# Kernel tuning notes

Hardware: AMD Instinct MI355X
Metric: run time of the kernel (lower is better)

The kernel has to match this reference:

```python
import jax, jax.numpy as jnp
import numpy as np

D = 500  # GRUCell hidden/input size (hardcoded in source)


def setup_inputs() -> dict:
    key = jax.random.key(0)
    k1, k2, k3, k4, k5 = jax.random.split(key, 5)
    B = 512
    bound = 1.0 / np.sqrt(D)  # torch GRUCell default uniform init bound
    state = jax.random.normal(k1, (B, D), dtype=jnp.float32)
    W_ih = jax.random.uniform(k2, (3 * D, D), jnp.float32, -bound, bound)
    W_hh = jax.random.uniform(k3, (3 * D, D), jnp.float32, -bound, bound)
    b_ih = jax.random.uniform(k4, (3 * D,), jnp.float32, -bound, bound)
    b_hh = jax.random.uniform(k5, (3 * D,), jnp.float32, -bound, bound)
    break_condition = jnp.float32(0.9)  # nn.Parameter(torch.tensor(0.9))
    recursion_limit = 64  # source uses 10000; reduced for a runnable baseline
    return {
        "state": state, "W_ih": W_ih, "W_hh": W_hh,
        "b_ih": b_ih, "b_hh": b_hh,
        "break_condition": break_condition,
        "recursion_limit": recursion_limit,
    }


def _gru_cell(x, h, W_ih, W_hh, b_ih, b_hh):
    # torch.nn.GRUCell math
    gi = x @ W_ih.T + b_ih          # [B, 3D]
    gh = h @ W_hh.T + b_hh          # [B, 3D]
    i_r, i_z, i_n = jnp.split(gi, 3, axis=-1)
    h_r, h_z, h_n = jnp.split(gh, 3, axis=-1)
    r = jax.nn.sigmoid(i_r + h_r)
    z = jax.nn.sigmoid(i_z + h_z)
    n = jnp.tanh(i_n + r * h_n)
    return (1.0 - z) * n + z * h


def reference(state, W_ih, W_hh, b_ih, b_hh, break_condition, recursion_limit):
    h0 = jnp.zeros_like(state)

    def step(carry, _):
        s, h, done = carry
        h_new = _gru_cell(s, h, W_ih, W_hh, b_ih, b_hh)
        done_new = done | (jnp.mean(h_new) > break_condition)
        # latch state/hidden once the break condition has fired
        s_out = jnp.where(done, s, h_new)
        h_out = jnp.where(done, h, h_new)
        return (s_out, h_out, done_new), None

    init = (state, h0, jnp.array(False))
    (s_fin, _, _), _ = jax.lax.scan(step, init, None, length=recursion_limit)
    return s_fin
```

## Files before the change

### kernel.cpp

```cpp
#include <hip/hip_runtime.h>
#include <math.h>
#include <stdint.h>

#define DD 500
#define BB 512
#define NSTRIPS 64
#define MSTRIPS 16
#define WKSTEPS 96
#define AKSTEPS 64
#define NELEM (BB*DD)
#define GM 16
#define GN 8
#define NBLK 128
#define HSTRIDE 2048

typedef _Float16 f16;
typedef _Float16 f16x8 __attribute__((ext_vector_type(8)));
typedef float    f32x16 __attribute__((ext_vector_type(16)));
typedef unsigned u32x4  __attribute__((ext_vector_type(4)));

#define APCNT ((size_t)MSTRIPS * AKSTEPS * 64 * 8)
#define WPCNT ((size_t)NSTRIPS * WKSTEPS * 64 * 8)


__device__ __forceinline__ float aload_f32(const float* p) {
    return __hip_atomic_load(p, __ATOMIC_RELAXED, __HIP_MEMORY_SCOPE_AGENT);
}
__device__ __forceinline__ void aload16i(u32x4& d, const f16* p) {
    asm volatile("global_load_dwordx4 %0, %1, off sc0 sc1"
                 : "=&v"(d) : "v"(p) : "memory");
}
__device__ __forceinline__ void astore16(f16* p, u32x4 v) {
    asm volatile("global_store_dwordx4 %0, %1, off sc0 sc1"
                 :: "v"(p), "v"(v) : "memory");
}

__device__ __forceinline__ float fsigmoid(float x) {
    return 1.0f / (1.0f + __expf(-x));
}
__device__ __forceinline__ float ftanh(float x) {
    return 2.0f / (1.0f + __expf(-2.0f * x)) - 1.0f;
}

__global__ __launch_bounds__(256) void conv_w(const float* __restrict__ Wih,
                                              const float* __restrict__ Whh,
                                              f16* __restrict__ Wp0,
                                              f16* __restrict__ Wp1)
{
    int p = blockIdx.x * 256 + threadIdx.x;
    const int ln = p & 63; p >>= 6;
    const int kstep = p % WKSTEPS;
    const int strip = p / WKSTEPS;
    const int q = ln & 31;
    const int g = q >> 3;
    const int d = strip * 8 + (q & 7);
    const int kb0 = kstep * 16 + (ln >> 5) * 8;
    const int blk = kb0 >> 9, bk0 = kb0 & 511;
    const float* pih = 0;
    const float* phh = 0;
    if (d < DD) {
        if (g == 0)      { pih = Wih + (size_t)d * DD;
                           phh = Whh + (size_t)d * DD; }
        else if (g == 1) { pih = Wih + (size_t)(500 + d) * DD;
                           phh = Whh + (size_t)(500 + d) * DD; }
        else if (g == 2) { pih = Wih + (size_t)(1000 + d) * DD; }
        else             { phh = Whh + (size_t)(1000 + d) * DD; }
    }
    f16 o0[8], o1[8];
    #pragma unroll
    for (int j = 0; j < 8; ++j) {
        const int bk = bk0 + j;
        float vi = 0.f, vh = 0.f;
        if (bk < DD) {
            if (pih) vi = pih[bk];
            if (phh) vh = phh[bk];
        }
        const float v0 = (g == 3) ? vh : vi;
        const float v1 = (g <= 1) ? (vi + vh) : v0;
        f16 h0 = (f16)v0;
        f16 h1 = (f16)v1;
        o0[j] = (blk == 2) ? (f16)(v0 - (float)h0) : h0;
        o1[j] = (blk == 2) ? (f16)(v1 - (float)h1) : h1;
    }
    const size_t off = ((size_t)(strip * WKSTEPS + kstep) * 64 + ln) * 8;
    *(uint4*)(Wp0 + off) = *(uint4*)o0;
    *(uint4*)(Wp1 + off) = *(uint4*)o1;
}

__global__ __launch_bounds__(256) void conv_a(const float* __restrict__ S,
                                              f16* __restrict__ Ap)
{
    int p = blockIdx.x * 256 + threadIdx.x;
    const int ln = p & 63; p >>= 6;
    const int kstep = p % AKSTEPS;
    const int strip = p / AKSTEPS;
    const int b = strip * 32 + (ln & 31);
    const int kb0 = kstep * 16 + (ln >> 5) * 8;
    const int blk = kb0 >> 9, bk0 = kb0 & 511;
    f16 out[8];
    #pragma unroll
    for (int j = 0; j < 8; ++j) {
        const int bk = bk0 + j;
        float v = (bk < DD) ? S[(size_t)b * DD + bk] : 0.f;
        f16 hi = (f16)v;
        out[j] = (blk == 1) ? (f16)(v - (float)hi) : hi;
    }
    *(uint4*)(Ap + ((size_t)(strip * AKSTEPS + kstep) * 64 + ln) * 8) = *(uint4*)out;
}

__device__ __forceinline__ void grid_sync(unsigned* bar, unsigned e)
{
    __syncthreads();
    if (threadIdx.x == 0) {
        unsigned* gcnt = bar + ((blockIdx.x >> 3) << 4);
        unsigned* root = bar + 512;
        unsigned* gen  = bar + 528;
        unsigned a = __hip_atomic_fetch_add(gcnt, 1u, __ATOMIC_RELAXED,
                                            __HIP_MEMORY_SCOPE_AGENT);
        if (a == e * 8u + 7u) {
            unsigned r = __hip_atomic_fetch_add(root, 1u, __ATOMIC_RELAXED,
                                                __HIP_MEMORY_SCOPE_AGENT);
            if (r == e * 16u + 15u) {
                __hip_atomic_store(gen, e + 1u, __ATOMIC_RELAXED,
                                   __HIP_MEMORY_SCOPE_AGENT);
            } else {
                while (__hip_atomic_load(gen, __ATOMIC_RELAXED,
                                         __HIP_MEMORY_SCOPE_AGENT) <= e)
                    __builtin_amdgcn_s_sleep(1);
            }
        } else {
            while (__hip_atomic_load(gen, __ATOMIC_RELAXED,
                                     __HIP_MEMORY_SCOPE_AGENT) <= e)
                __builtin_amdgcn_s_sleep(1);
        }
    }
    __syncthreads();
}

__global__ __launch_bounds__(512, 2) void gru_persist(
    f16* __restrict__ ApB,
    const f16* __restrict__ Wp0, const f16* __restrict__ Wp1,
    const float* __restrict__ bih, const float* __restrict__ bhh,
    float* __restrict__ out, float* __restrict__ spart,
    const float* __restrict__ bc, const int* __restrict__ rec,
    unsigned* __restrict__ bar, unsigned* __restrict__ garr,
    float* __restrict__ hist)
{
    const int bid = blockIdx.x;
    const int tid = threadIdx.x;
    const int rounds = min(64, rec[0]);
    if (rounds <= 0) return;
    const float thr = bc[0] * (float)NELEM;

    const int cg = bid & 7;
    const int mg = bid >> 3;
    const int wv = tid >> 6, ln = tid & 63;
    const int pp = wv & 3;
    const int kh = wv >> 2;
    const int ks0 = kh * 48;
    const int sb0 = cg * 8 + 2 * pp, sb1 = sb0 + 1;

    __shared__ __align__(16) char smem[65536];
    f16*      Alds  = (f16*)smem;
    float*    Ct    = (float*)smem;
    unsigned* hbufP = (unsigned*)(smem + 40960);
    float*    red   = (float*)(smem + 49408);
    int*      trig  = (int*)(smem + 49440);

    float h[4];
    #pragma unroll
    for (int i = 0; i < 4; ++i) h[i] = 0.0f;

    f16* bufs0 = ApB;
    f16* bufs1 = ApB + APCNT;
    unsigned* gptr = garr + mg * 16;
    unsigned wep = 0;

    for (int t = 0; t < rounds; ++t) {
        const f16* Wb   = (t == 0) ? Wp0 : Wp1;
        const f16* Bp0  = Wb + (size_t)(sb0 * WKSTEPS + ks0) * 512 + (size_t)ln * 8;
        const f16* Bp1  = Wb + (size_t)(sb1 * WKSTEPS + ks0) * 512 + (size_t)ln * 8;
        const f16* Asrc = ((t & 1) ? bufs1 : bufs0) + (size_t)mg * AKSTEPS * 512;
        f16*       Apw  = ((t & 1) ? bufs0 : bufs1);

        uint4 rB0[12], rB1[12];
        #pragma unroll
        for (int i = 0; i < 12; ++i) {
            rB0[i] = *(const uint4*)(Bp0 + (size_t)i * 512);
            rB1[i] = *(const uint4*)(Bp1 + (size_t)i * 512);
        }
        if (t > 0) {
            if (tid == 0) {
                while (__hip_atomic_load(gptr, __ATOMIC_RELAXED,
                                         __HIP_MEMORY_SCOPE_AGENT)
                       < 8u * (unsigned)t)
                    __builtin_amdgcn_s_sleep(1);
            }
            __syncthreads();
        }

        {
            u32x4 av[8];
            #pragma unroll
            for (int i = 0; i < 8; ++i)
                aload16i(av[i], Asrc + (size_t)(tid + 512 * i) * 8);
            asm volatile("s_waitcnt vmcnt(0)" ::: "memory");
            __builtin_amdgcn_sched_barrier(0);
            #pragma unroll
            for (int i = 0; i < 8; ++i)
                *(u32x4*)(Alds + (size_t)(tid + 512 * i) * 8) = av[i];
        }
        __syncthreads();

        f32x16 acc0 = {}, acc1 = {};
        #pragma unroll
        for (int ksl = 0; ksl < 48; ++ksl) {
            const int ks = ks0 + ksl;
            const int kr = (ks < 64) ? ks : (ks - 64);
            f16x8 a = *(const f16x8*)(Alds + (size_t)(kr * 64 + ln) * 8);
            acc0 = __builtin_amdgcn_mfma_f32_32x32x16_f16(
                       a, *(f16x8*)&rB0[ksl % 12], acc0, 0, 0, 0);
            acc1 = __builtin_amdgcn_mfma_f32_32x32x16_f16(
                       a, *(f16x8*)&rB1[ksl % 12], acc1, 0, 0, 0);
            if (ksl < 36) {
                rB0[ksl % 12] = *(const uint4*)(Bp0 + (size_t)(ksl + 12) * 512);
                rB1[ksl % 12] = *(const uint4*)(Bp1 + (size_t)(ksl + 12) * 512);
            }
        }
        __syncthreads();

        {
            const int q = ln & 31, g = q >> 3, dd = q & 7;
            const int sl0 = 2 * pp, sl1 = 2 * pp + 1;
            if (kh == 0) {
                #pragma unroll
                for (int r = 0; r < 16; ++r) {
                    const int row = (r & 3) + 8 * (r >> 2) + 4 * (ln >> 5);
                    Ct[row * 288 + sl0 * 36 + g * 9 + dd] = acc0[r];
                    Ct[row * 288 + sl1 * 36 + g * 9 + dd] = acc1[r];
                }
            }
            __syncthreads();
            if (kh == 1) {
                #pragma unroll
                for (int r = 0; r < 16; ++r) {
                    const int row = (r & 3) + 8 * (r >> 2) + 4 * (ln >> 5);
                    Ct[row * 288 + sl0 * 36 + g * 9 + dd] += acc0[r];
                    Ct[row * 288 + sl1 * 36 + g * 9 + dd] += acc1[r];
                }
            }
            __syncthreads();
        }

        float* hw = hist + ((size_t)bid * 8 + (size_t)(t & 7)) * HSTRIDE;
        float psum = 0.0f;
        #pragma unroll
        for (int i = 0; i < 4; ++i) {
            const int idx = i * 512 + tid;
            const int row = idx >> 6, dl = idx & 63;
            const int d = cg * 64 + dl;
            const int sl = dl >> 3, dd = dl & 7;
            float hnew = 0.0f;
            if (d < DD) {
                const float* cb = &Ct[row * 288 + sl * 36 + dd];
                float cr = cb[0], cz = cb[9], cin = cb[18], chn = cb[27];
                float r = fsigmoid(cr + bih[d] + bhh[d]);
                float z = fsigmoid(cz + bih[500 + d] + bhh[500 + d]);
                float inn = cin + bih[1000 + d];
                float hn  = bhh[1000 + d];
                float hp  = 0.0f;
                if (t > 0) { hn += chn; hp = h[i]; }
                float n = ftanh(inn + r * hn);
                hnew = (1.0f - z) * n + z * hp;
                psum += hnew;
            }
            h[i] = hnew;
            hw[idx] = hnew;
            f16 hi = (f16)hnew;
            f16 lo = (f16)(hnew - (float)hi);
            union { f16 f[2]; unsigned u; } pk;
            pk.f[0] = hi; pk.f[1] = lo;
            hbufP[row * 65 + dl] = pk.u;
        }
        #pragma unroll
        for (int off = 32; off > 0; off >>= 1) psum += __shfl_down(psum, off, 64);
        if (ln == 0) red[wv] = psum;
        __syncthreads();
        if (tid == 0) {
            float v = red[0] + red[1] + red[2] + red[3]
                    + red[4] + red[5] + red[6] + red[7];
            __hip_atomic_fetch_add(&spart[(size_t)cg * 64 + t], v,
                                   __ATOMIC_RELAXED, __HIP_MEMORY_SCOPE_AGENT);
        }
        if (tid < 256) {
            const int lm = tid & 31, oct = tid >> 5;
            union { f16 a[8]; u32x4 v; } hiU, loU;
            #pragma unroll
            for (int j = 0; j < 8; ++j) {
                unsigned u = hbufP[lm * 65 + oct * 8 + j];
                union { unsigned u; f16 f[2]; } pk; pk.u = u;
                hiU.a[j] = pk.f[0];
                loU.a[j] = pk.f[1];
            }
            const int kst = cg * 4 + (oct >> 1), half = oct & 1;
            f16* dhi = Apw + ((size_t)(mg * AKSTEPS + kst)      * 64 + half * 32 + lm) * 8;
            f16* dlo = Apw + ((size_t)(mg * AKSTEPS + 32 + kst) * 64 + half * 32 + lm) * 8;
            astore16(dhi, hiU.v);
            astore16(dlo, loU.v);
        }
        asm volatile("s_waitcnt vmcnt(0)" ::: "memory");
        __syncthreads();
        if (tid == 0)
            __hip_atomic_fetch_add(gptr, 1u, __ATOMIC_RELAXED,
                                   __HIP_MEMORY_SCOPE_AGENT);

        if (((t & 7) == 7) || (t == rounds - 1)) {
            grid_sync(bar, wep++);
            if (tid < 64) {
                const int cgl = tid & 7, ti = tid >> 3;
                const int tt = (t & ~7) + ti;
                float v = 0.f;
                if (tt <= t)
                    v = aload_f32(&spart[(size_t)cgl * 64 + tt]);
                v += __shfl_xor(v, 1, 64);
                v += __shfl_xor(v, 2, 64);
                v += __shfl_xor(v, 4, 64);
                bool hit = ((tid & 7) == 0) && (tt <= t) && (v > thr);
                unsigned long long m = __ballot(hit);
                if (tid == 0)
                    trig[0] = m ? (int)((__ffsll((long long)m) - 1) >> 3) : -1;
            }
            __syncthreads();
            const int w0 = trig[0];
            if (w0 >= 0) {
                const int ts = (t & ~7) + w0;
                const float* hs = hist
                    + ((size_t)bid * 8 + (size_t)(ts & 7)) * HSTRIDE;
                #pragma unroll
                for (int i = 0; i < 4; ++i) {
                    const int idx = i * 512 + tid;
                    const int row = idx >> 6, dl = idx & 63;
                    const int d = cg * 64 + dl;
                    if (d < DD)
                        out[(size_t)(mg * 32 + row) * DD + d] = hs[idx];
                }
                return;
            }
        }
    }

    #pragma unroll
    for (int i = 0; i < 4; ++i) {
        const int idx = i * 512 + tid;
        const int row = idx >> 6, dl = idx & 63;
        const int d = cg * 64 + dl;
        if (d < DD)
            out[(size_t)(mg * 32 + row) * DD + d] = h[i];
    }
}

extern "C" void kernel_launch(void* const* d_in, const int* in_sizes, int n_in,
                              void* d_out, int out_size, void* d_ws, size_t ws_size,
                              hipStream_t stream)
{
    const float* state = (const float*)d_in[0];
    const float* Wih   = (const float*)d_in[1];
    const float* Whh   = (const float*)d_in[2];
    const float* bih   = (const float*)d_in[3];
    const float* bhh   = (const float*)d_in[4];
    const float* bc    = (const float*)d_in[5];
    const int*   rec   = (const int*)d_in[6];

    char* ws = (char*)d_ws;
    float*    spart = (float*)ws;
    unsigned* bar   = (unsigned*)(ws + 2048);
    unsigned* garr  = (unsigned*)(ws + 6144);
    f16*   ApB   = (f16*)(ws + 8192);
    f16*   Wp0   = ApB + 2 * APCNT;
    f16*   Wp1   = Wp0 + WPCNT;
    float* hist  = (float*)(Wp1 + WPCNT);
    float* out   = (float*)d_out;

    hipMemsetAsync(ws, 0, 8192, stream);
    hipMemcpyAsync(out, state, (size_t)NELEM * sizeof(float),
                   hipMemcpyDeviceToDevice, stream);

    conv_w<<<dim3(NSTRIPS * WKSTEPS * 64 / 256), 256, 0, stream>>>(Wih, Whh, Wp0, Wp1);
    conv_a<<<dim3(MSTRIPS * AKSTEPS * 64 / 256), 256, 0, stream>>>(state, ApB);

    gru_persist<<<dim3(NBLK), dim3(512), 0, stream>>>(
        ApB, Wp0, Wp1, bih, bhh, out, spart, bc, rec, bar, garr, hist);
}
```

Measured before the change: 803.4 us.

## Repartition persistent GRU grid to 256 blocks with 64-row by 16-column tiles

Changes the persistent kernel's work split from 128 blocks (32 rows × 64 hidden columns, K split in two halves) to 256 blocks (64 rows × 16 hidden columns, K split four ways across waves). Each block now keeps fewer weight strips in registers and loads its A operand in two staged halves through LDS, overlapping the second half's global load with the first half's MFMAs. The aim is to put more CUs to work per recurrent step and shorten per-step latency. The cost is a wider grid barrier and row-group counter (32 arrivals instead of 8), four serialized LDS reduction passes, and more duplicated A traffic per block.

```diff
diff --git a/kernel.cpp b/kernel.cpp
--- a/kernel.cpp
+++ b/kernel.cpp
@@ -9,10 +9,10 @@
 #define WKSTEPS 96
 #define AKSTEPS 64
 #define NELEM (BB*DD)
-#define GM 16
-#define GN 8
-#define NBLK 128
-#define HSTRIDE 2048
+#define GRG 8
+#define GCG 32
+#define NBLK 256
+#define HSTRIDE 1024
 
 typedef _Float16 f16;
 typedef _Float16 f16x8 __attribute__((ext_vector_type(8)));
@@ -120,7 +120,7 @@
         if (a == e * 8u + 7u) {
             unsigned r = __hip_atomic_fetch_add(root, 1u, __ATOMIC_RELAXED,
                                                 __HIP_MEMORY_SCOPE_AGENT);
-            if (r == e * 16u + 15u) {
+            if (r == e * 32u + 31u) {
                 __hip_atomic_store(gen, e + 1u, __ATOMIC_RELAXED,
                                    __HIP_MEMORY_SCOPE_AGENT);
             } else {
@@ -152,117 +152,146 @@
     if (rounds <= 0) return;
     const float thr = bc[0] * (float)NELEM;
 
-    const int cg = bid & 7;
-    const int mg = bid >> 3;
+    const int cg = bid & 31;
+    const int rg = bid >> 5;
     const int wv = tid >> 6, ln = tid & 63;
-    const int pp = wv & 3;
-    const int kh = wv >> 2;
-    const int ks0 = kh * 48;
-    const int sb0 = cg * 8 + 2 * pp, sb1 = sb0 + 1;
+    const int mh = wv >> 2;
+    const int kq = wv & 3;
+    const int sb0 = cg * 2, sb1 = cg * 2 + 1;
 
     __shared__ __align__(16) char smem[65536];
     f16*      Alds  = (f16*)smem;
     float*    Ct    = (float*)smem;
-    unsigned* hbufP = (unsigned*)(smem + 40960);
-    float*    red   = (float*)(smem + 49408);
-    int*      trig  = (int*)(smem + 49440);
-
-    float h[4];
-    #pragma unroll
-    for (int i = 0; i < 4; ++i) h[i] = 0.0f;
+    unsigned* hbufP = (unsigned*)(smem + 20480);
+    float*    red   = (float*)(smem + 24832);
+    int*      trig  = (int*)(smem + 24864);
+
+    float h[2];
+    h[0] = 0.0f; h[1] = 0.0f;
 
     f16* bufs0 = ApB;
     f16* bufs1 = ApB + APCNT;
-    unsigned* gptr = garr + mg * 16;
+    unsigned* gptr = garr + rg * 16;
     unsigned wep = 0;
 
     for (int t = 0; t < rounds; ++t) {
-        const f16* Wb   = (t == 0) ? Wp0 : Wp1;
-        const f16* Bp0  = Wb + (size_t)(sb0 * WKSTEPS + ks0) * 512 + (size_t)ln * 8;
-        const f16* Bp1  = Wb + (size_t)(sb1 * WKSTEPS + ks0) * 512 + (size_t)ln * 8;
-        const f16* Asrc = ((t & 1) ? bufs1 : bufs0) + (size_t)mg * AKSTEPS * 512;
-        f16*       Apw  = ((t & 1) ? bufs0 : bufs1);
-
-        uint4 rB0[12], rB1[12];
-        #pragma unroll
-        for (int i = 0; i < 12; ++i) {
-            rB0[i] = *(const uint4*)(Bp0 + (size_t)i * 512);
-            rB1[i] = *(const uint4*)(Bp1 + (size_t)i * 512);
+        const f16* Wb    = (t == 0) ? Wp0 : Wp1;
+        const f16* Abase = (t & 1) ? bufs1 : bufs0;
+        f16*       Apw   = (t & 1) ? bufs0 : bufs1;
+        const f16* Bb0   = Wb + (size_t)sb0 * WKSTEPS * 512 + (size_t)ln * 8;
+        const f16* Bb1   = Wb + (size_t)sb1 * WKSTEPS * 512 + (size_t)ln * 8;
+
+        uint4 rB0[8], rB1[8];
+        #pragma unroll
+        for (int i = 0; i < 8; ++i) {
+            rB0[i] = *(const uint4*)(Bb0 + (size_t)(kq * 8 + i) * 512);
+            rB1[i] = *(const uint4*)(Bb1 + (size_t)(kq * 8 + i) * 512);
         }
         if (t > 0) {
             if (tid == 0) {
                 while (__hip_atomic_load(gptr, __ATOMIC_RELAXED,
                                          __HIP_MEMORY_SCOPE_AGENT)
-                       < 8u * (unsigned)t)
+                       < 32u * (unsigned)t)
                     __builtin_amdgcn_s_sleep(1);
             }
             __syncthreads();
         }
 
-        {
-            u32x4 av[8];
-            #pragma unroll
-            for (int i = 0; i < 8; ++i)
-                aload16i(av[i], Asrc + (size_t)(tid + 512 * i) * 8);
-            asm volatile("s_waitcnt vmcnt(0)" ::: "memory");
-            __builtin_amdgcn_sched_barrier(0);
-            #pragma unroll
-            for (int i = 0; i < 8; ++i)
-                *(u32x4*)(Alds + (size_t)(tid + 512 * i) * 8) = av[i];
+        u32x4 av[8];
+        #pragma unroll
+        for (int i = 0; i < 8; ++i) {
+            const int flat = tid + 512 * i;
+            const int sl_ = flat >> 11, rem = flat & 2047;
+            aload16i(av[i], Abase +
+                ((size_t)((2 * rg + sl_) * AKSTEPS + (rem >> 6)) * 64
+                 + (rem & 63)) * 8);
+        }
+        asm volatile("s_waitcnt vmcnt(0)" ::: "memory");
+        __builtin_amdgcn_sched_barrier(0);
+        #pragma unroll
+        for (int i = 0; i < 8; ++i)
+            *(u32x4*)(Alds + (size_t)(tid + 512 * i) * 8) = av[i];
+        #pragma unroll
+        for (int i = 0; i < 8; ++i) {
+            const int flat = tid + 512 * i;
+            const int sl_ = flat >> 11, rem = flat & 2047;
+            aload16i(av[i], Abase +
+                ((size_t)((2 * rg + sl_) * AKSTEPS + 32 + (rem >> 6)) * 64
+                 + (rem & 63)) * 8);
         }
         __syncthreads();
 
         f32x16 acc0 = {}, acc1 = {};
         #pragma unroll
-        for (int ksl = 0; ksl < 48; ++ksl) {
-            const int ks = ks0 + ksl;
-            const int kr = (ks < 64) ? ks : (ks - 64);
-            f16x8 a = *(const f16x8*)(Alds + (size_t)(kr * 64 + ln) * 8);
+        for (int ksl = 0; ksl < 16; ++ksl) {
+            const int ka = kq * 8 + (ksl & 7);
+            f16x8 a = *(const f16x8*)(Alds + ((size_t)(mh * 32 + ka) * 512
+                                              + (size_t)ln * 8));
             acc0 = __builtin_amdgcn_mfma_f32_32x32x16_f16(
-                       a, *(f16x8*)&rB0[ksl % 12], acc0, 0, 0, 0);
+                       a, *(f16x8*)&rB0[ksl & 7], acc0, 0, 0, 0);
             acc1 = __builtin_amdgcn_mfma_f32_32x32x16_f16(
-                       a, *(f16x8*)&rB1[ksl % 12], acc1, 0, 0, 0);
-            if (ksl < 36) {
-                rB0[ksl % 12] = *(const uint4*)(Bp0 + (size_t)(ksl + 12) * 512);
-                rB1[ksl % 12] = *(const uint4*)(Bp1 + (size_t)(ksl + 12) * 512);
-            }
+                       a, *(f16x8*)&rB1[ksl & 7], acc1, 0, 0, 0);
+            if (ksl < 8) {
+                rB0[ksl] = *(const uint4*)(Bb0 + (size_t)(64 + kq * 8 + ksl) * 512);
+                rB1[ksl] = *(const uint4*)(Bb1 + (size_t)(64 + kq * 8 + ksl) * 512);
+            }
+        }
+        __syncthreads();
+
+        asm volatile("s_waitcnt vmcnt(0)" ::: "memory");
+        __builtin_amdgcn_sched_barrier(0);
+        #pragma unroll
+        for (int i = 0; i < 8; ++i)
+            *(u32x4*)(Alds + (size_t)(tid + 512 * i) * 8) = av[i];
+        #pragma unroll
+        for (int i = 0; i < 8; ++i) {
+            rB0[i] = *(const uint4*)(Bb0 + (size_t)(32 + kq * 8 + i) * 512);
+            rB1[i] = *(const uint4*)(Bb1 + (size_t)(32 + kq * 8 + i) * 512);
+        }
+        __syncthreads();
+
+        #pragma unroll
+        for (int ksl = 0; ksl < 8; ++ksl) {
+            const int ka = kq * 8 + ksl;
+            f16x8 a = *(const f16x8*)(Alds + ((size_t)(mh * 32 + ka) * 512
+                                              + (size_t)ln * 8));
+            acc0 = __builtin_amdgcn_mfma_f32_32x32x16_f16(
+                       a, *(f16x8*)&rB0[ksl], acc0, 0, 0, 0);
+            acc1 = __builtin_amdgcn_mfma_f32_32x32x16_f16(
+                       a, *(f16x8*)&rB1[ksl], acc1, 0, 0, 0);
         }
         __syncthreads();
 
         {
             const int q = ln & 31, g = q >> 3, dd = q & 7;
-            const int sl0 = 2 * pp, sl1 = 2 * pp + 1;
-            if (kh == 0) {
-                #pragma unroll
-                for (int r = 0; r < 16; ++r) {
-                    const int row = (r & 3) + 8 * (r >> 2) + 4 * (ln >> 5);
-                    Ct[row * 288 + sl0 * 36 + g * 9 + dd] = acc0[r];
-                    Ct[row * 288 + sl1 * 36 + g * 9 + dd] = acc1[r];
+            #pragma unroll
+            for (int k = 0; k < 4; ++k) {
+                if (kq == k) {
+                    #pragma unroll
+                    for (int r = 0; r < 16; ++r) {
+                        const int row = mh * 32 + (r & 3) + 8 * (r >> 2)
+                                        + 4 * (ln >> 5);
+                        float* c0 = Ct + row * 72 + g * 9 + dd;
+                        float* c1 = c0 + 36;
+                        if (k == 0) { *c0 = acc0[r];  *c1 = acc1[r]; }
+                        else        { *c0 += acc0[r]; *c1 += acc1[r]; }
+                    }
                 }
-            }
-            __syncthreads();
-            if (kh == 1) {
-                #pragma unroll
-                for (int r = 0; r < 16; ++r) {
-                    const int row = (r & 3) + 8 * (r >> 2) + 4 * (ln >> 5);
-                    Ct[row * 288 + sl0 * 36 + g * 9 + dd] += acc0[r];
-                    Ct[row * 288 + sl1 * 36 + g * 9 + dd] += acc1[r];
-                }
-            }
-            __syncthreads();
+                __syncthreads();
+            }
         }
 
         float* hw = hist + ((size_t)bid * 8 + (size_t)(t & 7)) * HSTRIDE;
         float psum = 0.0f;
         #pragma unroll
-        for (int i = 0; i < 4; ++i) {
+        for (int i = 0; i < 2; ++i) {
             const int idx = i * 512 + tid;
-            const int row = idx >> 6, dl = idx & 63;
-            const int d = cg * 64 + dl;
+            const int row = idx >> 4, dl = idx & 15;
+            const int d = cg * 16 + dl;
             const int sl = dl >> 3, dd = dl & 7;
             float hnew = 0.0f;
             if (d < DD) {
-                const float* cb = &Ct[row * 288 + sl * 36 + dd];
+                const float* cb = &Ct[row * 72 + sl * 36 + dd];
                 float cr = cb[0], cz = cb[9], cin = cb[18], chn = cb[27];
                 float r = fsigmoid(cr + bih[d] + bhh[d]);
                 float z = fsigmoid(cz + bih[500 + d] + bhh[500 + d]);
@@ -280,7 +309,7 @@
             f16 lo = (f16)(hnew - (float)hi);
             union { f16 f[2]; unsigned u; } pk;
             pk.f[0] = hi; pk.f[1] = lo;
-            hbufP[row * 65 + dl] = pk.u;
+            hbufP[row * 17 + dl] = pk.u;
         }
         #pragma unroll
         for (int off = 32; off > 0; off >>= 1) psum += __shfl_down(psum, off, 64);
@@ -289,22 +318,24 @@
         if (tid == 0) {
             float v = red[0] + red[1] + red[2] + red[3]
                     + red[4] + red[5] + red[6] + red[7];
-            __hip_atomic_fetch_add(&spart[(size_t)cg * 64 + t], v,
+            __hip_atomic_fetch_add(&spart[(size_t)(cg & 7) * 64 + t], v,
                                    __ATOMIC_RELAXED, __HIP_MEMORY_SCOPE_AGENT);
         }
-        if (tid < 256) {
-            const int lm = tid & 31, oct = tid >> 5;
+        if (tid < 128) {
+            const int row = tid >> 1, oct = tid & 1;
             union { f16 a[8]; u32x4 v; } hiU, loU;
             #pragma unroll
             for (int j = 0; j < 8; ++j) {
-                unsigned u = hbufP[lm * 65 + oct * 8 + j];
+                unsigned u = hbufP[row * 17 + oct * 8 + j];
                 union { unsigned u; f16 f[2]; } pk; pk.u = u;
                 hiU.a[j] = pk.f[0];
                 loU.a[j] = pk.f[1];
             }
-            const int kst = cg * 4 + (oct >> 1), half = oct & 1;
-            f16* dhi = Apw + ((size_t)(mg * AKSTEPS + kst)      * 64 + half * 32 + lm) * 8;
-            f16* dlo = Apw + ((size_t)(mg * AKSTEPS + 32 + kst) * 64 + half * 32 + lm) * 8;
+            const int strip = 2 * rg + (row >> 5), lm = row & 31;
+            f16* dhi = Apw + ((size_t)(strip * AKSTEPS + cg)      * 64
+                              + oct * 32 + lm) * 8;
+            f16* dlo = Apw + ((size_t)(strip * AKSTEPS + 32 + cg) * 64
+                              + oct * 32 + lm) * 8;
             astore16(dhi, hiU.v);
             astore16(dlo, loU.v);
         }
@@ -337,12 +368,12 @@
                 const float* hs = hist
                     + ((size_t)bid * 8 + (size_t)(ts & 7)) * HSTRIDE;
                 #pragma unroll
-                for (int i = 0; i < 4; ++i) {
+                for (int i = 0; i < 2; ++i) {
                     const int idx = i * 512 + tid;
-                    const int row = idx >> 6, dl = idx & 63;
-                    const int d = cg * 64 + dl;
+                    const int row = idx >> 4, dl = idx & 15;
+                    const int d = cg * 16 + dl;
                     if (d < DD)
-                        out[(size_t)(mg * 32 + row) * DD + d] = hs[idx];
+                        out[(size_t)(rg * 64 + row) * DD + d] = hs[idx];
                 }
                 return;
             }
@@ -350,12 +381,12 @@
     }
 
     #pragma unroll
-    for (int i = 0; i < 4; ++i) {
+    for (int i = 0; i < 2; ++i) {
         const int idx = i * 512 + tid;
-        const int row = idx >> 6, dl = idx & 63;
-        const int d = cg * 64 + dl;
+        const int row = idx >> 4, dl = idx & 15;
+        const int d = cg * 16 + dl;
         if (d < DD)
-            out[(size_t)(mg * 32 + row) * DD + d] = h[i];
+            out[(size_t)(rg * 64 + row) * DD + d] = h[i];
     }
 }
 
```

Result: faster. 690.8 us (median of 2 runs) (-14.0%).
